# Performance work log

Measured on AMD Instinct MI355X. Metric: run time of the kernel, lower is better.

Reference implementation:

```python
import jax, jax.numpy as jnp
import numpy as np

N_HEADS = 16
HEAD_DIM = 64
THRESHOLD = 0.5
TAU = 12.5
N_FHN_STEPS = 2


def fhn_imex_step(v, w, I, a, b, dt, tau):
    # IMEX step of FitzHugh-Nagumo dynamics:
    #   explicit update for v (nonlinear), implicit for w (linear in w)
    #   dv/dt = v - v^3/3 - w + I
    #   dw/dt = (v + a - b*w) / tau
    v_new = v + dt * (v - v ** 3 / 3.0 - w + I)
    w_new = (w + (dt / tau) * (v_new + a)) / (1.0 + (dt / tau) * b)
    return v_new, w_new


def setup_inputs() -> dict:
    key = jax.random.key(0)
    k1, k2, k3 = jax.random.split(key, 3)
    B, T, D = 2, 2048, 1024
    x = jax.random.normal(k1, (B, T, D), dtype=jnp.float32)
    Wqkv = jax.random.normal(k2, (3 * D, D), dtype=jnp.float32) * 0.02
    Wout = jax.random.normal(k3, (D, D), dtype=jnp.float32) * 0.02
    a = jnp.float32(0.7)
    b = jnp.float32(0.8)
    dt = jnp.float32(1.0)
    return {"x": x, "Wqkv": Wqkv, "Wout": Wout, "a": a, "b": b, "dt": dt}


def reference(x, Wqkv, Wout, a, b, dt):
    B, T, D = x.shape
    H, hd = N_HEADS, HEAD_DIM
    qkv = x @ Wqkv.T                              # (B, T, 3D)
    qkv = qkv.reshape(B, T, 3, H, hd)             # 'b t (three h d)'
    q = qkv[:, :, 0].transpose(0, 2, 1, 3)        # (B, H, T, hd)
    k = qkv[:, :, 1].transpose(0, 2, 1, 3)
    v = qkv[:, :, 2].transpose(0, 2, 1, 3)

    scores = jnp.einsum('bhtd,bhsd->bhts', q, k) / np.sqrt(hd).astype(np.float32)
    causal = jnp.triu(jnp.ones((T, T), dtype=bool), k=1)
    scores = jnp.where(causal[None, None], -jnp.inf, scores)
    attn_probs = jax.nn.softmax(scores, axis=-1)  # (B, H, T, T); dropout=0 -> identity

    attn_energy = attn_probs.sum(axis=-1)                              # (B, H, T)
    stim_scale = jnp.maximum(jnp.abs(attn_energy).max(axis=-1, keepdims=True), 1e-6)
    stimulus_normed = attn_energy / stim_scale
    threshold_gate = jax.nn.sigmoid((jnp.abs(attn_energy) - THRESHOLD) * 10.0)
    I = stimulus_normed * (0.1 + 0.9 * threshold_gate)                 # (B, H, T)
    I = jnp.broadcast_to(I[..., None], (B, H, T, hd))                  # expand to head_dim

    v_state = jnp.zeros_like(I)
    w_state = jnp.zeros_like(I)
    for _ in range(N_FHN_STEPS):
        v_state, w_state = fhn_imex_step(v_state, w_state, I, a, b, dt, TAU)

    fhn_gate = jax.nn.sigmoid(v_state.mean(axis=-1))[..., None]        # (B, H, T, 1)
    attn_probs = attn_probs * (0.5 + 0.5 * fhn_gate)
    attn_probs = attn_probs / (attn_probs.sum(axis=-1, keepdims=True) + 1e-8)

    out = jnp.einsum('bhts,bhsd->bhtd', attn_probs, v)                 # (B, H, T, hd)
    out = out.transpose(0, 2, 1, 3).reshape(B, T, D)
    out = out @ Wout.T
    return out
```

## Files before the change

kernel.cpp:

```cpp
#include <hip/hip_runtime.h>

typedef unsigned short u16;
typedef __attribute__((ext_vector_type(8))) short bf16x8;
typedef __attribute__((ext_vector_type(4))) float f32x4;
typedef __attribute__((ext_vector_type(4))) unsigned short u16x4;
typedef __attribute__((ext_vector_type(2))) unsigned short u16x2;

__device__ __forceinline__ u16 f2bf(float f) {
    unsigned int u = __builtin_bit_cast(unsigned int, f);
    u += 0x7fffu + ((u >> 16) & 1u);
    return (u16)(u >> 16);
}

__device__ __forceinline__ float bf2f(u16 b) {
    unsigned int u = ((unsigned int)b) << 16;
    return __builtin_bit_cast(float, u);
}

__device__ __forceinline__ void gload_lds16(const u16* g, const u16* l) {
    __builtin_amdgcn_global_load_lds((const __attribute__((address_space(1))) void*)g,
                                     (__attribute__((address_space(3))) void*)l,
                                     16, 0, 0);
}

__global__ __launch_bounds__(256) void cvt_f32_bf16(const float* __restrict__ in,
                                                    u16* __restrict__ out, int n4) {
    int i = blockIdx.x * blockDim.x + threadIdx.x;
    int stride = gridDim.x * blockDim.x;
    for (; i < n4; i += stride) {
        float4 v = reinterpret_cast<const float4*>(in)[i];
        u16x4 o = { f2bf(v.x), f2bf(v.y), f2bf(v.z), f2bf(v.w) };
        reinterpret_cast<u16x4*>(out)[i] = o;
    }
}

template <typename OutT>
__global__ __launch_bounds__(256) void gemm_bt(const u16* __restrict__ A, const u16* __restrict__ B,
                                               OutT* __restrict__ C, int M, int N, int K) {
    __shared__ u16 ldsA[128 * 64];
    __shared__ u16 ldsB[128 * 64];
    const int tid = threadIdx.x;
    const int lane = tid & 63;
    const int wid = tid >> 6;
    const int wm = wid >> 1, wn = wid & 1;
    const int lq = lane & 15, lg = lane >> 4;
    const int bm = blockIdx.y * 128, bn = blockIdx.x * 128;

    const u16* aSrc[4];
    const u16* bSrc[4];
    int dstOff[4];
#pragma unroll
    for (int j = 0; j < 4; ++j) {
        int item = j * 256 + tid;
        int row = item >> 3;
        int c16 = item & 7;
        aSrc[j] = A + (size_t)(bm + row) * K + c16 * 8;
        bSrc[j] = B + (size_t)(bn + row) * K + c16 * 8;
        dstOff[j] = (j * 256 + (tid & ~63)) * 16;
    }

    f32x4 acc[4][4] = {};
    for (int k0 = 0; k0 < K; k0 += 64) {
        if (k0) __syncthreads();
#pragma unroll
        for (int j = 0; j < 4; ++j) {
            gload_lds16(aSrc[j], (const u16*)((const char*)ldsA + dstOff[j]));
            gload_lds16(bSrc[j], (const u16*)((const char*)ldsB + dstOff[j]));
            aSrc[j] += 64;
            bSrc[j] += 64;
        }
        __syncthreads();
#pragma unroll
        for (int kk = 0; kk < 2; ++kk) {
            bf16x8 af[4], bfr[4];
#pragma unroll
            for (int m = 0; m < 4; ++m) {
                int row = wm * 64 + m * 16 + lq;
                af[m] = *(const bf16x8*)((const char*)ldsA + row * 128 + kk * 64 + lg * 16);
            }
#pragma unroll
            for (int n = 0; n < 4; ++n) {
                int row = wn * 64 + n * 16 + lq;
                bfr[n] = *(const bf16x8*)((const char*)ldsB + row * 128 + kk * 64 + lg * 16);
            }
#pragma unroll
            for (int m = 0; m < 4; ++m)
#pragma unroll
                for (int n = 0; n < 4; ++n)
                    acc[m][n] = __builtin_amdgcn_mfma_f32_16x16x32_bf16(af[m], bfr[n], acc[m][n], 0, 0, 0);
        }
    }

#pragma unroll
    for (int m = 0; m < 4; ++m) {
#pragma unroll
        for (int n = 0; n < 4; ++n) {
#pragma unroll
            for (int r = 0; r < 4; ++r) {
                int row = bm + wm * 64 + m * 16 + lg * 4 + r;
                int col = bn + wn * 64 + n * 16 + lq;
                float v = acc[m][n][r];
                if constexpr (sizeof(OutT) == 2)
                    C[(size_t)row * N + col] = (OutT)f2bf(v);
                else
                    C[(size_t)row * N + col] = (OutT)v;
            }
        }
    }
}

__global__ __launch_bounds__(256) void transpose_v(const u16* __restrict__ qkv, u16* __restrict__ vt) {
    __shared__ u16 tile[64][72];
    const int tb = blockIdx.x * 64;
    const int bh = blockIdx.y;
    const int b = bh >> 4, h = bh & 15;
    const u16* src = qkv + ((size_t)(b * 2048 + tb)) * 3072 + 2048 + h * 64;
    const int tid = threadIdx.x;
#pragma unroll
    for (int p = 0; p < 2; ++p) {
        int item = p * 256 + tid;
        int t = item >> 3, c = item & 7;
        bf16x8 v = *(const bf16x8*)(src + (size_t)t * 3072 + c * 8);
        *(bf16x8*)(&tile[t][c * 8]) = v;
    }
    __syncthreads();
    u16* dst = vt + ((size_t)bh * 64) * 2048 + tb;
#pragma unroll
    for (int p = 0; p < 2; ++p) {
        int item = p * 256 + tid;
        int d = item >> 3, tc = item & 7;
        bf16x8 o;
#pragma unroll
        for (int j = 0; j < 8; ++j) o[j] = (short)tile[tc * 8 + j][d];
        *(bf16x8*)(dst + (size_t)d * 2048 + tc * 8) = o;
    }
}

__global__ __launch_bounds__(256, 4) void fhn_attn(const u16* __restrict__ qkv, const u16* __restrict__ vt,
                                                   u16* __restrict__ attno) {
    __shared__ u16 kvbuf[2][2][64 * 64];
    __shared__ u16 plds[4][16][64];
    const int bh = blockIdx.y;
    const int qt = (bh < 16) ? (31 - (int)blockIdx.x) : (int)blockIdx.x;
    const int b = bh >> 4, h = bh & 15;
    const int tid = threadIdx.x;
    const int w = tid >> 6;
    const int lane = tid & 63;
    const int lq = lane & 15, lg = lane >> 4;
    const int qlo = qt * 64 + w * 16;
    const int tq = qlo + lq;

    bf16x8 qf[2];
    {
        const u16* qrow = qkv + ((size_t)(b * 2048 + tq)) * 3072 + h * 64;
        qf[0] = *(const bf16x8*)(qrow + lg * 8);
        qf[1] = *(const bf16x8*)(qrow + 32 + lg * 8);
#pragma unroll
        for (int kk = 0; kk < 2; ++kk)
#pragma unroll
            for (int j = 0; j < 8; ++j)
                qf[kk][j] = (short)f2bf(bf2f((u16)qf[kk][j]) * 0.1803368801f);
    }

    const int it0 = tid, it1 = 256 + tid;
    const int r0 = it0 >> 3, g0 = (it0 & 7) ^ (r0 & 7);
    const int r1 = it1 >> 3, g1 = (it1 & 7) ^ (r1 & 7);
    const u16* kS0 = qkv + ((size_t)(b * 2048 + r0)) * 3072 + 1024 + h * 64 + g0 * 8;
    const u16* kS1 = qkv + ((size_t)(b * 2048 + r1)) * 3072 + 1024 + h * 64 + g1 * 8;
    const u16* vS0 = vt + ((size_t)bh * 64 + r0) * 2048 + g0 * 8;
    const u16* vS1 = vt + ((size_t)bh * 64 + r1) * 2048 + g1 * 8;
    const int d0 = (it0 & ~63) * 8;
    const int d1 = (it1 & ~63) * 8;

#define STAGE(buf)                                            \
    do {                                                      \
        gload_lds16(kS0, &kvbuf[buf][0][d0]);                 \
        gload_lds16(kS1, &kvbuf[buf][0][d1]);                 \
        gload_lds16(vS0, &kvbuf[buf][1][d0]);                 \
        gload_lds16(vS1, &kvbuf[buf][1][d1]);                 \
        kS0 += 64 * 3072; kS1 += 64 * 3072;                   \
        vS0 += 64; vS1 += 64;                                 \
    } while (0)

    const int nkv = qt + 1;
    float m_run = -1e30f, l_run = 0.f;
    f32x4 oacc[4] = {};
    int cur = 0;

    char* const pbase = (char*)&plds[w][0][0] + lq * 128;
    const int pswz = (lq & 7) << 4;

    STAGE(0);

    for (int jb = 0; jb < nkv; ++jb) {
        if (jb + 1 < nkv) {
            STAGE(cur ^ 1);
            asm volatile("s_waitcnt vmcnt(4)" ::: "memory");
        } else {
            asm volatile("s_waitcnt vmcnt(0)" ::: "memory");
        }
        __builtin_amdgcn_s_barrier();
        __builtin_amdgcn_sched_barrier(0);

        const u16* kb = kvbuf[cur][0];
        const u16* vb = kvbuf[cur][1];

        float p[4][4];
#pragma unroll
        for (int st = 0; st < 4; ++st) {
            int row = st * 16 + lq;
            f32x4 sacc = {};
            sacc = __builtin_amdgcn_mfma_f32_16x16x32_bf16(
                *(const bf16x8*)(kb + row * 64 + ((lg ^ (row & 7)) * 8)), qf[0], sacc, 0, 0, 0);
            sacc = __builtin_amdgcn_mfma_f32_16x16x32_bf16(
                *(const bf16x8*)(kb + row * 64 + (((4 + lg) ^ (row & 7)) * 8)), qf[1], sacc, 0, 0, 0);
#pragma unroll
            for (int r = 0; r < 4; ++r) p[st][r] = sacc[r];
        }

        if (jb == qt) {
#pragma unroll
            for (int st = 0; st < 4; ++st)
#pragma unroll
                for (int r = 0; r < 4; ++r) {
                    int s = jb * 64 + st * 16 + lg * 4 + r;
                    if (s > tq) p[st][r] = -1e30f;
                }
        }

        float mloc = p[0][0];
#pragma unroll
        for (int st = 0; st < 4; ++st)
#pragma unroll
            for (int r = 0; r < 4; ++r) mloc = fmaxf(mloc, p[st][r]);
        mloc = fmaxf(mloc, __shfl_xor(mloc, 16));
        mloc = fmaxf(mloc, __shfl_xor(mloc, 32));

        if (!__all(mloc - m_run <= 8.0f)) {
            float mnew = fmaxf(m_run, mloc);
            float scp = exp2f(m_run - mnew);
            m_run = mnew;
            l_run *= scp;
            float f0 = __shfl(scp, lg * 4 + 0);
            float f1 = __shfl(scp, lg * 4 + 1);
            float f2_ = __shfl(scp, lg * 4 + 2);
            float f3 = __shfl(scp, lg * 4 + 3);
#pragma unroll
            for (int nd = 0; nd < 4; ++nd) {
                oacc[nd][0] *= f0; oacc[nd][1] *= f1;
                oacc[nd][2] *= f2_; oacc[nd][3] *= f3;
            }
        }

        float lloc = 0.f;
#pragma unroll
        for (int st = 0; st < 4; ++st)
#pragma unroll
            for (int r = 0; r < 4; ++r) {
                float e = exp2f(p[st][r] - m_run);
                p[st][r] = e;
                lloc += e;
            }
        lloc += __shfl_xor(lloc, 16);
        lloc += __shfl_xor(lloc, 32);
        l_run += lloc;

#pragma unroll
        for (int st = 0; st < 4; ++st) {
            u16x4 pk = { f2bf(p[st][0]), f2bf(p[st][1]), f2bf(p[st][2]), f2bf(p[st][3]) };
            *(u16x4*)(pbase + ((st * 32 + lg * 8) ^ pswz)) = pk;
        }

#pragma unroll
        for (int c = 0; c < 2; ++c) {
            bf16x8 pa = *(const bf16x8*)(pbase + ((c * 64 + lg * 16) ^ pswz));
#pragma unroll
            for (int nd = 0; nd < 4; ++nd) {
                int row = nd * 16 + lq;
                bf16x8 vf = *(const bf16x8*)(vb + row * 64 + (((c * 4 + lg) ^ (row & 7)) * 8));
                oacc[nd] = __builtin_amdgcn_mfma_f32_16x16x32_bf16(pa, vf, oacc[nd], 0, 0, 0);
            }
        }

        __builtin_amdgcn_sched_barrier(0);
        __builtin_amdgcn_s_barrier();
        cur ^= 1;
    }
#undef STAGE

    float li0 = 1.f / __shfl(l_run, lg * 4 + 0);
    float li1 = 1.f / __shfl(l_run, lg * 4 + 1);
    float li2 = 1.f / __shfl(l_run, lg * 4 + 2);
    float li3 = 1.f / __shfl(l_run, lg * 4 + 3);
#pragma unroll
    for (int nd = 0; nd < 4; ++nd) {
#pragma unroll
        for (int r = 0; r < 4; ++r) {
            int trow = qlo + lg * 4 + r;
            float li = (r == 0) ? li0 : (r == 1) ? li1 : (r == 2) ? li2 : li3;
            attno[((size_t)(b * 2048 + trow)) * 1024 + h * 64 + nd * 16 + lq] =
                f2bf(oacc[nd][r] * li);
        }
    }
}

extern "C" void kernel_launch(void* const* d_in, const int* in_sizes, int n_in,
                              void* d_out, int out_size, void* d_ws, size_t ws_size,
                              hipStream_t stream) {
    const float* x    = (const float*)d_in[0];
    const float* Wqkv = (const float*)d_in[1];
    const float* Wout = (const float*)d_in[2];
    float* out = (float*)d_out;

    char* ws = (char*)d_ws;
    u16* xb    = (u16*)(ws + 0);
    u16* wqkvb = (u16*)(ws + 8388608);
    u16* woutb = (u16*)(ws + 14680064);
    u16* qkvb  = (u16*)(ws + 16777216);
    u16* vtb   = (u16*)(ws + 41943040);
    u16* attno = (u16*)(ws + 50331648);

    cvt_f32_bf16<<<2048, 256, 0, stream>>>(x, xb, 4194304 / 4);
    cvt_f32_bf16<<<2048, 256, 0, stream>>>(Wqkv, wqkvb, 3145728 / 4);
    cvt_f32_bf16<<<1024, 256, 0, stream>>>(Wout, woutb, 1048576 / 4);

    gemm_bt<u16><<<dim3(24, 32), 256, 0, stream>>>(xb, wqkvb, qkvb, 4096, 3072, 1024);

    transpose_v<<<dim3(32, 32), 256, 0, stream>>>(qkvb, vtb);

    fhn_attn<<<dim3(32, 32), 256, 0, stream>>>(qkvb, vtb, attno);

    gemm_bt<float><<<dim3(8, 32), 256, 0, stream>>>(attno, woutb, out, 4096, 1024, 1024);
}
```

Baseline: 132.1 us.

## Remap attention grid, add MFMA priority hints, packed bf16 convert, tree reductions

The attention kernel now runs on a 1D grid. Each block id maps to a (batch-head, tile) pair so that consecutive blocks cover different heads and alternate long and short causal tiles, which should balance work across XCDs and CUs. The MFMA sections are wrapped in s_setprio raises, the softmax conversion uses the hardware v_cvt_pk_bf16_f32 instruction fused into the exp loop, and the max and sum reductions become trees to shorten dependency chains. The risks are small rounding differences from the hardware conversion and a less predictable schedule.

```diff
diff --git a/kernel.cpp b/kernel.cpp
--- a/kernel.cpp
+++ b/kernel.cpp
@@ -4,7 +4,7 @@
 typedef __attribute__((ext_vector_type(8))) short bf16x8;
 typedef __attribute__((ext_vector_type(4))) float f32x4;
 typedef __attribute__((ext_vector_type(4))) unsigned short u16x4;
-typedef __attribute__((ext_vector_type(2))) unsigned short u16x2;
+typedef __attribute__((ext_vector_type(2))) unsigned int u32x2;
 
 __device__ __forceinline__ u16 f2bf(float f) {
     unsigned int u = __builtin_bit_cast(unsigned int, f);
@@ -15,6 +15,12 @@
 __device__ __forceinline__ float bf2f(u16 b) {
     unsigned int u = ((unsigned int)b) << 16;
     return __builtin_bit_cast(float, u);
+}
+
+__device__ __forceinline__ unsigned int cvt_pk_bf16(float lo, float hi) {
+    unsigned int r;
+    asm("v_cvt_pk_bf16_f32 %0, %1, %2" : "=v"(r) : "v"(lo), "v"(hi));
+    return r;
 }
 
 __device__ __forceinline__ void gload_lds16(const u16* g, const u16* l) {
@@ -140,8 +146,10 @@
                                                    u16* __restrict__ attno) {
     __shared__ u16 kvbuf[2][2][64 * 64];
     __shared__ u16 plds[4][16][64];
-    const int bh = blockIdx.y;
-    const int qt = (bh < 16) ? (31 - (int)blockIdx.x) : (int)blockIdx.x;
+    const int id = blockIdx.x;
+    const int bh = (id & 7) * 4 + ((id >> 3) & 3);
+    const int tile = id >> 5;
+    const int qt = (bh & 1) ? tile : (31 - tile);
     const int b = bh >> 4, h = bh & 15;
     const int tid = threadIdx.x;
     const int w = tid >> 6;
@@ -206,6 +214,7 @@
         const u16* vb = kvbuf[cur][1];
 
         float p[4][4];
+        __builtin_amdgcn_s_setprio(1);
 #pragma unroll
         for (int st = 0; st < 4; ++st) {
             int row = st * 16 + lq;
@@ -217,6 +226,7 @@
 #pragma unroll
             for (int r = 0; r < 4; ++r) p[st][r] = sacc[r];
         }
+        __builtin_amdgcn_s_setprio(0);
 
         if (jb == qt) {
 #pragma unroll
@@ -228,11 +238,11 @@
                 }
         }
 
-        float mloc = p[0][0];
+        float mst[4];
 #pragma unroll
         for (int st = 0; st < 4; ++st)
-#pragma unroll
-            for (int r = 0; r < 4; ++r) mloc = fmaxf(mloc, p[st][r]);
+            mst[st] = fmaxf(fmaxf(p[st][0], p[st][1]), fmaxf(p[st][2], p[st][3]));
+        float mloc = fmaxf(fmaxf(mst[0], mst[1]), fmaxf(mst[2], mst[3]));
         mloc = fmaxf(mloc, __shfl_xor(mloc, 16));
         mloc = fmaxf(mloc, __shfl_xor(mloc, 32));
 
@@ -252,25 +262,22 @@
             }
         }
 
-        float lloc = 0.f;
-#pragma unroll
-        for (int st = 0; st < 4; ++st)
-#pragma unroll
-            for (int r = 0; r < 4; ++r) {
-                float e = exp2f(p[st][r] - m_run);
-                p[st][r] = e;
-                lloc += e;
-            }
+        float lst[4];
+#pragma unroll
+        for (int st = 0; st < 4; ++st) {
+#pragma unroll
+            for (int r = 0; r < 4; ++r)
+                p[st][r] = exp2f(p[st][r] - m_run);
+            lst[st] = (p[st][0] + p[st][1]) + (p[st][2] + p[st][3]);
+            u32x2 pk = { cvt_pk_bf16(p[st][0], p[st][1]), cvt_pk_bf16(p[st][2], p[st][3]) };
+            *(u32x2*)(pbase + ((st * 32 + lg * 8) ^ pswz)) = pk;
+        }
+        float lloc = (lst[0] + lst[1]) + (lst[2] + lst[3]);
         lloc += __shfl_xor(lloc, 16);
         lloc += __shfl_xor(lloc, 32);
         l_run += lloc;
 
-#pragma unroll
-        for (int st = 0; st < 4; ++st) {
-            u16x4 pk = { f2bf(p[st][0]), f2bf(p[st][1]), f2bf(p[st][2]), f2bf(p[st][3]) };
-            *(u16x4*)(pbase + ((st * 32 + lg * 8) ^ pswz)) = pk;
-        }
-
+        __builtin_amdgcn_s_setprio(1);
 #pragma unroll
         for (int c = 0; c < 2; ++c) {
             bf16x8 pa = *(const bf16x8*)(pbase + ((c * 64 + lg * 16) ^ pswz));
@@ -281,6 +288,7 @@
                 oacc[nd] = __builtin_amdgcn_mfma_f32_16x16x32_bf16(pa, vf, oacc[nd], 0, 0, 0);
             }
         }
+        __builtin_amdgcn_s_setprio(0);
 
         __builtin_amdgcn_sched_barrier(0);
         __builtin_amdgcn_s_barrier();
@@ -328,7 +336,7 @@
 
     transpose_v<<<dim3(32, 32), 256, 0, stream>>>(qkvb, vtb);
 
-    fhn_attn<<<dim3(32, 32), 256, 0, stream>>>(qkvb, vtb, attno);
+    fhn_attn<<<1024, 256, 0, stream>>>(qkvb, vtb, attno);
 
     gemm_bt<float><<<dim3(8, 32), 256, 0, stream>>>(attno, woutb, out, 4096, 1024, 1024);
 }
```

Result: no change. 131.8 us (-0.2%).
